# Optimization experiments

Measured on AMD Instinct MI355X. Metric: run time of the kernel, lower is better.

The kernel has to match this reference:

```python
import jax, jax.numpy as jnp
from jax import lax
import numpy as np

B, NUM_TPM, NUM_CNV, NODE_DIM, DRUG_FEAT = 32, 16000, 16000, 36, 75
N_DRUGS, N_ATOMS, N_PAIRS = 128, 64, 4096


def setup_inputs() -> dict:
    key = jax.random.key(0)
    ks = jax.random.split(key, 32)

    def w(k, shape):
        fan_in = shape[0] if len(shape) == 2 else int(np.prod(shape[1:]))
        return (jax.random.normal(k, shape, jnp.float32) / np.float32(np.sqrt(fan_in))).astype(jnp.float32)

    pic_dim = jax.random.normal(ks[0], (B, 3, 256, 256), jnp.float32)
    rna_seq = jax.random.normal(ks[1], (B, NUM_TPM), jnp.float32)
    gene_cnv = jax.random.normal(ks[2], (B, NUM_CNV), jnp.float32)
    drug_fea = jax.random.uniform(ks[3], (N_DRUGS, N_ATOMS, DRUG_FEAT), jnp.float32)
    a = (jax.random.uniform(ks[4], (N_DRUGS, N_ATOMS, N_ATOMS)) < 0.15).astype(jnp.float32)
    drug_adj = jnp.maximum(a, jnp.transpose(a, (0, 2, 1)))
    index_list = jnp.stack([
        jax.random.randint(ks[5], (N_PAIRS,), 0, B),
        jax.random.randint(ks[6], (N_PAIRS,), 0, N_DRUGS)], axis=1)
    target = jax.random.randint(ks[7], (N_PAIRS,), 0, 2)
    logit_scale = jnp.asarray(10.0, jnp.float32)
    return dict(
        pic_dim=pic_dim, rna_seq=rna_seq, gene_cnv=gene_cnv,
        drug_fea=drug_fea, drug_adj=drug_adj, index_list=index_list,
        target=target, logit_scale=logit_scale,
        conv_w=w(ks[8], (32, 3, 5, 5)), conv_b=jnp.zeros((32,), jnp.float32),
        fc1_w=w(ks[9], (32 * 128 * 128, 1024)), fc1_b=jnp.zeros((1024,), jnp.float32),
        fc2_w=w(ks[10], (1024, 36)), fc2_b=jnp.zeros((36,), jnp.float32),
        mlp1_w1=w(ks[11], (NUM_TPM, NUM_TPM // 4)), mlp1_b1=jnp.zeros((NUM_TPM // 4,), jnp.float32),
        mlp1_w2=w(ks[12], (NUM_TPM // 4, NODE_DIM)), mlp1_b2=jnp.zeros((NODE_DIM,), jnp.float32),
        mlp2_w1=w(ks[13], (NUM_CNV, NUM_CNV // 4)), mlp2_b1=jnp.zeros((NUM_CNV // 4,), jnp.float32),
        mlp2_w2=w(ks[14], (NUM_CNV // 4, NODE_DIM)), mlp2_b2=jnp.zeros((NODE_DIM,), jnp.float32),
        att_w1=w(ks[15], (36, 128)), att_b1=jnp.zeros((128,), jnp.float32),
        att_w2=w(ks[16], (128, 1)),
        end_w1=w(ks[17], (NODE_DIM * 4, NODE_DIM)), end_b1=jnp.zeros((NODE_DIM,), jnp.float32),
        end_w2=w(ks[18], (NODE_DIM, 2)), end_b2=jnp.zeros((2,), jnp.float32),
        gcn_w=w(ks[19], (DRUG_FEAT, NODE_DIM * 8)), gcn_w2=w(ks[20], (NODE_DIM * 8, NODE_DIM * 2)))


def _mlp(x, w1, b1, w2, b2):  # Linear-ReLU-(Dropout eval)-Linear-Softmax
    h = jax.nn.relu(x @ w1 + b1)
    return jax.nn.softmax(h @ w2 + b2, axis=-1)


def _ce(logits, labels):  # mean cross entropy, labels int [N]
    lp = jax.nn.log_softmax(logits, axis=-1)
    return -jnp.take_along_axis(lp, labels[:, None], axis=1).mean()


def reference(pic_dim, rna_seq, gene_cnv, drug_fea, drug_adj, index_list, target,
              logit_scale, conv_w, conv_b, fc1_w, fc1_b, fc2_w, fc2_b,
              mlp1_w1, mlp1_b1, mlp1_w2, mlp1_b2, mlp2_w1, mlp2_b1, mlp2_w2, mlp2_b2,
              att_w1, att_b1, att_w2, end_w1, end_b1, end_w2, end_b2, gcn_w, gcn_w2):
    # omics branches
    rna1 = _mlp(rna_seq, mlp1_w1, mlp1_b1, mlp1_w2, mlp1_b2)    # [B,36]
    cnv1 = _mlp(gene_cnv, mlp2_w1, mlp2_b1, mlp2_w2, mlp2_b2)   # [B,36]
    # image branch: conv(3->32,k5,p2) + relu + maxpool2 + fc
    x = lax.conv_general_dilated(pic_dim, conv_w, (1, 1), [(2, 2), (2, 2)])
    x = jax.nn.relu(x + conv_b[None, :, None, None])
    x = lax.reduce_window(x, -jnp.inf, lax.max, (1, 1, 2, 2), (1, 1, 2, 2), 'VALID')
    x = x.reshape(x.shape[0], -1)                               # [B, 32*128*128]
    x = jax.nn.relu(x @ fc1_w + fc1_b)
    pic1 = x @ fc2_w + fc2_b                                    # [B,36]
    # semantic attention over the two omics views
    z = jnp.stack([rna1, cnv1], axis=1)                         # [B,2,36]
    wv = (jnp.tanh(z @ att_w1 + att_b1) @ att_w2).mean(0)       # [2,1]
    beta = jax.nn.softmax(wv, axis=0)
    cell = (beta[None] * z).sum(1)                              # [B,36]
    # CLIP-style loss
    pic1 = pic1 / jnp.linalg.norm(pic1, axis=1, keepdims=True)
    cell = cell / jnp.linalg.norm(cell, axis=1, keepdims=True)
    image_fea = logit_scale * (pic1 @ cell.T)
    labels = jnp.arange(image_fea.shape[0])
    total_loss2 = (_ce(image_fea, labels) + _ce(image_fea.T, labels)) / 2
    cell_cat = jnp.concatenate([cell, pic1], axis=1)            # [B,72]
    # batched drug GCN (replaces per-drug python loop)
    eye = jnp.eye(N_ATOMS, dtype=jnp.float32)
    def gcn_one(X, A):
        Ht = A.T * (1.0 - eye) + eye        # set diagonal to 1 (add self loops)
        deg = Ht.sum(1)
        dinv = jnp.where(deg == 0, 0.0, 1.0 / deg)
        Hn = dinv[:, None] * Ht             # D^-1 A_hat  (== H.t() after norm)
        out = Hn @ ((Hn @ (X @ gcn_w)) @ gcn_w2)
        return jnp.max(jax.nn.relu(out), axis=0)  # max over atoms -> [72]
    drugfea = jax.vmap(gcn_one)(drug_fea, drug_adj)             # [n_drugs,72]
    # pair prediction head
    Bc = jnp.concatenate([cell_cat[index_list[:, 0]], drugfea[index_list[:, 1]]], axis=1)
    Bp = _mlp(Bc, end_w1, end_b1, end_w2, end_b2)               # [n_pairs,2]
    loss1 = _ce(Bp, target)
    return (loss1, total_loss2, Bp, target)
```

## Files before the change

### kernel.cpp

```cpp
#include <hip/hip_runtime.h>
#include <hip/hip_bf16.h>
#include <math.h>

typedef float evf4 __attribute__((ext_vector_type(4)));

__device__ __forceinline__ void fma4(float4& a, float s, const float4& v) {
  a.x += s * v.x; a.y += s * v.y; a.z += s * v.z; a.w += s * v.w;
}
__device__ __forceinline__ void fadd4(float4& a, const float4& v) {
  a.x += v.x; a.y += v.y; a.z += v.z; a.w += v.w;
}
__device__ __forceinline__ float4 ntload4(const float4* p) {
  evf4 v = __builtin_nontemporal_load((const evf4*)p);
  return make_float4(v.x, v.y, v.z, v.w);
}

__device__ __forceinline__ void conv_body(
    const float* __restrict__ pic, const float* __restrict__ cw,
    const float* __restrict__ cb, float* __restrict__ pooled,
    int bid, float tile[3][8][260]) {
  int php = bid & 63, ocg2 = (bid >> 6) & 1, b = bid >> 7;
  int tid = threadIdx.x;
  int pw = tid & 127, phl = tid >> 7;
  int ph = php * 2 + phl;
  int h_base = php * 4 - 2;
  for (int i = tid; i < 3 * 8 * 260; i += 256) {
    int c = i % 260; int rr = (i / 260) & 7; int ic = i / (260 * 8);
    int h = h_base + rr, w = c - 2;
    float v = 0.f;
    if (h >= 0 && h < 256 && w >= 0 && w < 256)
      v = pic[((size_t)b * 3 + ic) * 65536 + h * 256 + w];
    tile[ic][rr][c] = v;
  }
  __syncthreads();
  float acc[16][4];
#pragma unroll
  for (int o = 0; o < 16; ++o)
#pragma unroll
    for (int q = 0; q < 4; ++q) acc[o][q] = 0.f;
  int r0 = phl * 2;
  int c0 = pw * 2;
#pragma unroll
  for (int ic = 0; ic < 3; ++ic) {
    float win[6][6];
#pragma unroll
    for (int r = 0; r < 6; ++r)
#pragma unroll
      for (int cc = 0; cc < 6; ++cc) win[r][cc] = tile[ic][r0 + r][c0 + cc];
#pragma unroll
    for (int o = 0; o < 16; ++o) {
      const float* __restrict__ wk = cw + ((ocg2 * 16 + o) * 3 + ic) * 25;
#pragma unroll
      for (int kh = 0; kh < 5; ++kh)
#pragma unroll
        for (int kw = 0; kw < 5; ++kw) {
          float wv = wk[kh * 5 + kw];
          acc[o][0] += win[kh][kw] * wv;
          acc[o][1] += win[kh][kw + 1] * wv;
          acc[o][2] += win[kh + 1][kw] * wv;
          acc[o][3] += win[kh + 1][kw + 1] * wv;
        }
    }
  }
#pragma unroll
  for (int o = 0; o < 16; ++o) {
    float m = fmaxf(fmaxf(acc[o][0], acc[o][1]), fmaxf(acc[o][2], acc[o][3]));
    m = fmaxf(m + cb[ocg2 * 16 + o], 0.f);
    pooled[(((size_t)b * 32 + ocg2 * 16 + o) * 128 + ph) * 128 + pw] = m;
  }
}

__device__ __forceinline__ void wc_body(
    const float* __restrict__ w1, const float* __restrict__ w2,
    float* __restrict__ wc, int bx) {
  int i = bx * 256 + threadIdx.x;
  if (i >= 75 * 72) return;
  int r = i / 72, c = i - r * 72;
  float s = 0.f;
  for (int k = 0; k < 288; ++k) s += w1[r * 288 + k] * w2[k * 72 + c];
  wc[i] = s;
}

__global__ __launch_bounds__(256) void k1_conv_wc_kernel(
    const float* __restrict__ pic, const float* __restrict__ cw,
    const float* __restrict__ cb, float* __restrict__ pooled,
    const float* __restrict__ gw, const float* __restrict__ gw2,
    float* __restrict__ wcb) {
  __shared__ float tile[3][8][260];
  int bid = blockIdx.x;
  if (bid < 4096) conv_body(pic, cw, cb, pooled, bid, tile);
  else            wc_body(gw, gw2, wcb, bid - 4096);
}

__device__ __forceinline__ void gemm32p_body(
    const float* __restrict__ X, const float* __restrict__ W,
    float* __restrict__ partial, int K, int N, int chunk,
    int bx, int split, float xs[128][36]) {
  int tid = threadIdx.x;
  int colv = bx * 256 + tid;
  int col0 = colv * 4;
  bool active = col0 < N;
  int k0 = split * chunk, k1 = min(k0 + chunk, K);
  size_t Nv = (size_t)(N >> 2);
  const float4* Wv = (const float4*)W;
  float4 acc[32];
#pragma unroll
  for (int b = 0; b < 32; ++b) acc[b] = make_float4(0.f, 0.f, 0.f, 0.f);

  float4 xpre[4];
#pragma unroll
  for (int j = 0; j < 4; ++j) {
    int idx = tid + j * 256;
    int b = idx >> 5, kk = (idx & 31) * 4;
    xpre[j] = *(const float4*)&X[(size_t)b * K + k0 + kk];
  }

  auto fmablk = [&](int kk, const float4& w4) {
    const float4* xr = (const float4*)xs[kk];
#pragma unroll
    for (int b4 = 0; b4 < 8; ++b4) {
      float4 xv = xr[b4];
      fma4(acc[b4 * 4 + 0], xv.x, w4);
      fma4(acc[b4 * 4 + 1], xv.y, w4);
      fma4(acc[b4 * 4 + 2], xv.z, w4);
      fma4(acc[b4 * 4 + 3], xv.w, w4);
    }
  };

  for (int kt = k0; kt < k1; kt += 128) {
    __syncthreads();
#pragma unroll
    for (int j = 0; j < 4; ++j) {
      int idx = tid + j * 256;
      int b = idx >> 5, kk = (idx & 31) * 4;
      xs[kk + 0][b] = xpre[j].x;
      xs[kk + 1][b] = xpre[j].y;
      xs[kk + 2][b] = xpre[j].z;
      xs[kk + 3][b] = xpre[j].w;
    }
    __syncthreads();
    if (kt + 128 < k1) {
#pragma unroll
      for (int j = 0; j < 4; ++j) {
        int idx = tid + j * 256;
        int b = idx >> 5, kk = (idx & 31) * 4;
        xpre[j] = *(const float4*)&X[(size_t)b * K + kt + 128 + kk];
      }
    }
    if (active) {
      const float4* wp = Wv + (size_t)kt * Nv + colv;
      float4 cur[8], nxt[8];
#pragma unroll
      for (int j = 0; j < 8; ++j) cur[j] = ntload4(wp + (size_t)j * Nv);
#pragma unroll 1
      for (int g = 0; g < 15; ++g) {
        const float4* wn = wp + 8 * Nv;
#pragma unroll
        for (int j = 0; j < 8; ++j) nxt[j] = ntload4(wn + (size_t)j * Nv);
        int kb = g * 8;
#pragma unroll
        for (int j = 0; j < 8; ++j) fmablk(kb + j, cur[j]);
#pragma unroll
        for (int j = 0; j < 8; ++j) cur[j] = nxt[j];
        wp = wn;
      }
#pragma unroll
      for (int j = 0; j < 8; ++j) fmablk(120 + j, cur[j]);
    }
  }
  if (active) {
    float* p = partial + (size_t)split * 32 * N + col0;
#pragma unroll
    for (int b = 0; b < 32; ++b) *(float4*)(p + (size_t)b * N) = acc[b];
  }
}

__global__ __launch_bounds__(256) void gemm_all_kernel(
    const float* __restrict__ pooled, const float* __restrict__ fc1w,
    float* __restrict__ pfc1,
    const float* __restrict__ rna, const float* __restrict__ m1w1, float* __restrict__ pm1,
    const float* __restrict__ cnv, const float* __restrict__ m2w1, float* __restrict__ pm2) {
  __shared__ float xs[128][36];
  int b = blockIdx.x;
  if (b < 512) {
    gemm32p_body(pooled, fc1w, pfc1, 524288, 1024, 1024, 0, b, xs);
  } else {
    int j = b - 512;
    int z = j / 252;
    int r = j % 252;
    int bx = r & 3, split = r >> 2;
    if (z == 0) gemm32p_body(rna, m1w1, pm1, 16000, 4000, 256, bx, split, xs);
    else        gemm32p_body(cnv, m2w1, pm2, 16000, 4000, 256, bx, split, xs);
  }
}

__device__ __forceinline__ void reduce_s1_body(
    const float* __restrict__ partial, float* __restrict__ p2,
    int bx, int sy) {
  int i = bx * 256 + threadIdx.x;
  const float4* p = (const float4*)partial + (size_t)(sy * 128) * 8192 + i;
  const size_t st = 8192;
  float4 s0 = make_float4(0, 0, 0, 0), s1 = s0, s2 = s0, s3 = s0;
  for (int sp = 0; sp < 128; sp += 4) {
    fadd4(s0, ntload4(p + (sp + 0) * st));
    fadd4(s1, ntload4(p + (sp + 1) * st));
    fadd4(s2, ntload4(p + (sp + 2) * st));
    fadd4(s3, ntload4(p + (sp + 3) * st));
  }
  float4 r;
  r.x = (s0.x + s1.x) + (s2.x + s3.x);
  r.y = (s0.y + s1.y) + (s2.y + s3.y);
  r.z = (s0.z + s1.z) + (s2.z + s3.z);
  r.w = (s0.w + s1.w) + (s2.w + s3.w);
  ((float4*)p2)[(size_t)sy * 8192 + i] = r;
}

__device__ __forceinline__ void reduce_mlp_body(
    const float* __restrict__ partial, const float* __restrict__ bias,
    float* __restrict__ out, int bx) {
  int i = bx * 256 + threadIdx.x;
  if (i >= 32000) return;
  const float4* p = (const float4*)partial + i;
  const size_t st = 32000;
  float4 s0 = make_float4(0, 0, 0, 0), s1 = s0, s2 = s0, s3 = s0;
  int sp = 0;
  for (; sp + 4 <= 63; sp += 4) {
    fadd4(s0, ntload4(p + (sp + 0) * st));
    fadd4(s1, ntload4(p + (sp + 1) * st));
    fadd4(s2, ntload4(p + (sp + 2) * st));
    fadd4(s3, ntload4(p + (sp + 3) * st));
  }
  for (; sp < 63; ++sp) fadd4(s0, ntload4(p + (size_t)sp * st));
  float4 bi = ((const float4*)bias)[i % 1000];
  float4 r;
  r.x = fmaxf(bi.x + (s0.x + s1.x) + (s2.x + s3.x), 0.f);
  r.y = fmaxf(bi.y + (s0.y + s1.y) + (s2.y + s3.y), 0.f);
  r.z = fmaxf(bi.z + (s0.z + s1.z) + (s2.z + s3.z), 0.f);
  r.w = fmaxf(bi.w + (s0.w + s1.w) + (s2.w + s3.w), 0.f);
  ((float4*)out)[i] = r;
}

__global__ __launch_bounds__(256) void k3_reduce_kernel(
    const float* __restrict__ pfc1, float* __restrict__ p2fc1,
    const float* __restrict__ pm1, const float* __restrict__ m1b1, float* __restrict__ h1,
    const float* __restrict__ pm2, const float* __restrict__ m2b1, float* __restrict__ h2) {
  int b = blockIdx.x;
  if (b < 128) {
    reduce_s1_body(pfc1, p2fc1, b & 31, b >> 5);
  } else {
    int idx = b - 128;
    if (idx < 125) reduce_mlp_body(pm1, m1b1, h1, idx);
    else           reduce_mlp_body(pm2, m2b1, h2, idx - 125);
  }
}

__device__ __forceinline__ void reduce_s2_body(
    const float* __restrict__ p2, const float* __restrict__ bias,
    float* __restrict__ out, int bx) {
  int i = bx * 256 + threadIdx.x;
  float4 a = ((const float4*)p2)[i];
  float4 b = ((const float4*)p2)[8192 + i];
  float4 c = ((const float4*)p2)[16384 + i];
  float4 d = ((const float4*)p2)[24576 + i];
  float4 bi = ((const float4*)bias)[i & 255];
  float4 r;
  r.x = fmaxf(bi.x + (a.x + b.x) + (c.x + d.x), 0.f);
  r.y = fmaxf(bi.y + (a.y + b.y) + (c.y + d.y), 0.f);
  r.z = fmaxf(bi.z + (a.z + b.z) + (c.z + d.z), 0.f);
  r.w = fmaxf(bi.w + (a.w + b.w) + (c.w + d.w), 0.f);
  ((float4*)out)[i] = r;
}

__device__ __forceinline__ void gcn_body(
    const float* __restrict__ Xg, const float* __restrict__ Ag,
    const float* __restrict__ Wc, float* __restrict__ drugfea, int d,
    float Hn[64][65], float Xs[64][75], float Wcs[75][72],
    float Ys[64][72], float Ts[64][72]) {
  int tid = threadIdx.x;
  const float* Ad = Ag + (size_t)d * 4096;
  const float* Xd = Xg + (size_t)d * 4800;
  for (int i = tid; i < 4096; i += 256) {
    int r = i & 63, c = i >> 6;
    Hn[r][c] = (r == c) ? 1.f : Ad[c * 64 + r];
  }
  for (int i = tid; i < 4800; i += 256) Xs[i / 75][i % 75] = Xd[i];
  for (int i = tid; i < 5400; i += 256) Wcs[i / 72][i % 72] = Wc[i];
  __syncthreads();
  if (tid < 64) {
    float s = 0.f;
    for (int c = 0; c < 64; ++c) s += Hn[tid][c];
    float inv = (s == 0.f) ? 0.f : 1.f / s;
    for (int c = 0; c < 64; ++c) Hn[tid][c] *= inv;
  }
  __syncthreads();
  int rb = tid >> 3, cb = tid & 7;
  int r0 = rb * 2, c0 = cb * 9;
  {
    float o0[9], o1[9];
#pragma unroll
    for (int j = 0; j < 9; ++j) { o0[j] = 0.f; o1[j] = 0.f; }
    for (int k = 0; k < 75; ++k) {
      float x0 = Xs[r0][k], x1 = Xs[r0 + 1][k];
#pragma unroll
      for (int j = 0; j < 9; ++j) {
        float w = Wcs[k][c0 + j];
        o0[j] += x0 * w; o1[j] += x1 * w;
      }
    }
#pragma unroll
    for (int j = 0; j < 9; ++j) { Ys[r0][c0 + j] = o0[j]; Ys[r0 + 1][c0 + j] = o1[j]; }
  }
  __syncthreads();
  {
    float o0[9], o1[9];
#pragma unroll
    for (int j = 0; j < 9; ++j) { o0[j] = 0.f; o1[j] = 0.f; }
    for (int k = 0; k < 64; ++k) {
      float x0 = Hn[r0][k], x1 = Hn[r0 + 1][k];
#pragma unroll
      for (int j = 0; j < 9; ++j) {
        float w = Ys[k][c0 + j];
        o0[j] += x0 * w; o1[j] += x1 * w;
      }
    }
#pragma unroll
    for (int j = 0; j < 9; ++j) { Ts[r0][c0 + j] = o0[j]; Ts[r0 + 1][c0 + j] = o1[j]; }
  }
  __syncthreads();
  {
    float o0[9], o1[9];
#pragma unroll
    for (int j = 0; j < 9; ++j) { o0[j] = 0.f; o1[j] = 0.f; }
    for (int k = 0; k < 64; ++k) {
      float x0 = Hn[r0][k], x1 = Hn[r0 + 1][k];
#pragma unroll
      for (int j = 0; j < 9; ++j) {
        float w = Ts[k][c0 + j];
        o0[j] += x0 * w; o1[j] += x1 * w;
      }
    }
#pragma unroll
    for (int j = 0; j < 9; ++j) {
      Ys[r0][c0 + j] = fmaxf(o0[j], 0.f);
      Ys[r0 + 1][c0 + j] = fmaxf(o1[j], 0.f);
    }
  }
  __syncthreads();
  if (tid < 72) {
    float m = Ys[0][tid];
    for (int i = 1; i < 64; ++i) m = fmaxf(m, Ys[i][tid]);
    drugfea[d * 72 + tid] = m;
  }
}

__global__ __launch_bounds__(256) void k4_s2_gcn_kernel(
    const float* __restrict__ p2fc1, const float* __restrict__ fc1_b,
    float* __restrict__ fcact,
    const float* __restrict__ Xg, const float* __restrict__ Ag,
    const float* __restrict__ wcb, float* __restrict__ drugfea) {
  __shared__ float Hn[64][65];
  __shared__ float Xs[64][75];
  __shared__ float Wcs[75][72];
  __shared__ float Ys[64][72];
  __shared__ float Ts[64][72];
  int b = blockIdx.x;
  if (b < 32) reduce_s2_body(p2fc1, fc1_b, fcact, b);
  else        gcn_body(Xg, Ag, wcb, drugfea, b - 32, Hn, Xs, Wcs, Ys, Ts);
}

__global__ __launch_bounds__(256) void lin36_all_kernel(
    const float* __restrict__ X0, const float* __restrict__ W0,
    const float* __restrict__ bi0, float* __restrict__ out0,
    const float* __restrict__ X1, const float* __restrict__ W1,
    const float* __restrict__ bi1, float* __restrict__ out1,
    const float* __restrict__ X2, const float* __restrict__ W2,
    const float* __restrict__ bi2, float* __restrict__ out2) {
  const float* X; const float* W; const float* bias; float* out; int K; bool do_sm;
  if (blockIdx.y == 0)      { X = X0; W = W0; bias = bi0; out = out0; K = 4000; do_sm = true; }
  else if (blockIdx.y == 1) { X = X1; W = W1; bias = bi1; out = out1; K = 4000; do_sm = true; }
  else                      { X = X2; W = W2; bias = bi2; out = out2; K = 1024; do_sm = false; }
  __shared__ float xs[4000];
  __shared__ float red[28][36];
  __shared__ float vals[36];
  __shared__ float mxv, smv;
  int b = blockIdx.x, tid = threadIdx.x;
  for (int i = tid; i < K; i += 256) xs[i] = X[(size_t)b * K + i];
  __syncthreads();
  if (tid < 252) {
    int c4 = tid % 9, g = tid / 9;
    const float4* W4 = (const float4*)W;
    float4 s = make_float4(0.f, 0.f, 0.f, 0.f);
    for (int k = g; k < K; k += 28) fma4(s, xs[k], W4[k * 9 + c4]);
    red[g][c4 * 4 + 0] = s.x; red[g][c4 * 4 + 1] = s.y;
    red[g][c4 * 4 + 2] = s.z; red[g][c4 * 4 + 3] = s.w;
  }
  __syncthreads();
  if (tid < 36) {
    float s = bias[tid];
    for (int g = 0; g < 28; ++g) s += red[g][tid];
    vals[tid] = s;
  }
  __syncthreads();
  if (do_sm) {
    if (tid == 0) {
      float m = -1e30f;
      for (int j = 0; j < 36; ++j) m = fmaxf(m, vals[j]);
      float e = 0.f;
      for (int j = 0; j < 36; ++j) e += expf(vals[j] - m);
      mxv = m; smv = e;
    }
    __syncthreads();
    if (tid < 36) out[b * 36 + tid] = expf(vals[tid] - mxv) / smv;
  } else {
    if (tid < 36) out[b * 36 + tid] = vals[tid];
  }
}

__global__ __launch_bounds__(256) void head_kernel(
    const float* __restrict__ rna1, const float* __restrict__ cnv1,
    const float* __restrict__ pic1r, const float* __restrict__ aw1,
    const float* __restrict__ ab1, const float* __restrict__ aw2,
    const float* __restrict__ scale_p, float* __restrict__ cell_cat,
    float* __restrict__ dout) {
  __shared__ float z[2][32][36];
  __shared__ float pic1n[32][36];
  __shared__ float celln[32][36];
  __shared__ float fea[32][32];
  __shared__ float wvp[64];
  __shared__ float beta0, beta1;
  __shared__ float rowl[32], coll[32];
  int tid = threadIdx.x;
  for (int i = tid; i < 1152; i += 256) {
    int b = i / 36, k = i - (i / 36) * 36;
    z[0][b][k] = rna1[i];
    z[1][b][k] = cnv1[i];
    pic1n[b][k] = pic1r[i];
  }
  __syncthreads();
  {
    int p = tid >> 2, sub = tid & 3;
    int b = p >> 1, v = p & 1;
    float s = 0.f;
    for (int h = sub; h < 128; h += 4) {
      float a = ab1[h];
      for (int k = 0; k < 36; ++k) a += z[v][b][k] * aw1[k * 128 + h];
      s += tanhf(a) * aw2[h];
    }
    s += __shfl_down(s, 1, 64);
    s += __shfl_down(s, 2, 64);
    if (sub == 0) wvp[p] = s;
  }
  __syncthreads();
  if (tid == 0) {
    float w0 = 0.f, w1 = 0.f;
    for (int b = 0; b < 32; ++b) { w0 += wvp[b * 2]; w1 += wvp[b * 2 + 1]; }
    w0 /= 32.f; w1 /= 32.f;
    float m = fmaxf(w0, w1);
    float e0 = expf(w0 - m), e1 = expf(w1 - m);
    beta0 = e0 / (e0 + e1); beta1 = e1 / (e0 + e1);
  }
  __syncthreads();
  for (int i = tid; i < 1152; i += 256) {
    int b = i / 36, k = i - (i / 36) * 36;
    celln[b][k] = beta0 * z[0][b][k] + beta1 * z[1][b][k];
  }
  __syncthreads();
  if (tid < 32) {
    float s = 0.f;
    for (int k = 0; k < 36; ++k) { float x = pic1n[tid][k]; s += x * x; }
    float inv = 1.f / sqrtf(s);
    for (int k = 0; k < 36; ++k) pic1n[tid][k] *= inv;
  } else if (tid < 64) {
    int b = tid - 32;
    float s = 0.f;
    for (int k = 0; k < 36; ++k) { float x = celln[b][k]; s += x * x; }
    float inv = 1.f / sqrtf(s);
    for (int k = 0; k < 36; ++k) celln[b][k] *= inv;
  }
  __syncthreads();
  for (int i = tid; i < 1152; i += 256) {
    int b = i / 36, k = i - (i / 36) * 36;
    cell_cat[b * 72 + k] = celln[b][k];
    cell_cat[b * 72 + 36 + k] = pic1n[b][k];
  }
  float sc = *scale_p;
  for (int t = tid; t < 1024; t += 256) {
    int i = t >> 5, j = t & 31;
    float s = 0.f;
    for (int k = 0; k < 36; ++k) s += pic1n[i][k] * celln[j][k];
    fea[i][j] = sc * s;
  }
  __syncthreads();
  if (tid < 32) {
    float m = -1e30f;
    for (int j = 0; j < 32; ++j) m = fmaxf(m, fea[tid][j]);
    float e = 0.f;
    for (int j = 0; j < 32; ++j) e += expf(fea[tid][j] - m);
    rowl[tid] = (logf(e) + m) - fea[tid][tid];
  } else if (tid < 64) {
    int j = tid - 32;
    float m = -1e30f;
    for (int i = 0; i < 32; ++i) m = fmaxf(m, fea[i][j]);
    float e = 0.f;
    for (int i = 0; i < 32; ++i) e += expf(fea[i][j] - m);
    coll[j] = (logf(e) + m) - fea[j][j];
  }
  __syncthreads();
  if (tid == 0) {
    float s1 = 0.f, s2 = 0.f;
    for (int i = 0; i < 32; ++i) { s1 += rowl[i]; s2 += coll[i]; }
    dout[1] = 0.5f * (s1 / 32.f + s2 / 32.f);
  }
}

__global__ __launch_bounds__(256) void pair_kernel(
    const float* __restrict__ cell_cat, const float* __restrict__ drugfea,
    const int* __restrict__ idx, const int* __restrict__ target,
    const float* __restrict__ w1, const float* __restrict__ b1,
    const float* __restrict__ w2, const float* __restrict__ b2,
    float* __restrict__ bp_out, float* __restrict__ tgt_out,
    float* __restrict__ blocksums) {
  __shared__ float w1s[144][36];
  __shared__ float ccs[32][73];
  __shared__ float dfs[128][73];
  __shared__ float w2s[72], b2s[2];
  __shared__ float lsum[256];
  int tid = threadIdx.x;
  {
    float4* dst = (float4*)&w1s[0][0];
    const float4* src = (const float4*)w1;
    for (int i = tid; i < 1296; i += 256) dst[i] = src[i];
  }
  for (int i = tid; i < 2304; i += 256) ccs[i / 72][i % 72] = cell_cat[i];
  for (int i = tid; i < 9216; i += 256) dfs[i / 72][i % 72] = drugfea[i];
  if (tid < 72) w2s[tid] = w2[tid];
  if (tid < 2) b2s[tid] = b2[tid];
  __syncthreads();
  int p = blockIdx.x * 256 + tid;
  int ci = idx[p * 2], dj = idx[p * 2 + 1];
  float4 h4[9];
  {
    const float4* bb = (const float4*)b1;
#pragma unroll
    for (int q = 0; q < 9; ++q) h4[q] = bb[q];
  }
  for (int k = 0; k < 72; ++k) {
    float x = ccs[ci][k];
    const float4* wr = (const float4*)&w1s[k][0];
#pragma unroll
    for (int q = 0; q < 9; ++q) fma4(h4[q], x, wr[q]);
  }
  for (int k = 0; k < 72; ++k) {
    float x = dfs[dj][k];
    const float4* wr = (const float4*)&w1s[72 + k][0];
#pragma unroll
    for (int q = 0; q < 9; ++q) fma4(h4[q], x, wr[q]);
  }
  float l0 = b2s[0], l1 = b2s[1];
#pragma unroll
  for (int q = 0; q < 9; ++q) {
    float hv;
    hv = fmaxf(h4[q].x, 0.f); l0 += hv * w2s[(q * 4 + 0) * 2]; l1 += hv * w2s[(q * 4 + 0) * 2 + 1];
    hv = fmaxf(h4[q].y, 0.f); l0 += hv * w2s[(q * 4 + 1) * 2]; l1 += hv * w2s[(q * 4 + 1) * 2 + 1];
    hv = fmaxf(h4[q].z, 0.f); l0 += hv * w2s[(q * 4 + 2) * 2]; l1 += hv * w2s[(q * 4 + 2) * 2 + 1];
    hv = fmaxf(h4[q].w, 0.f); l0 += hv * w2s[(q * 4 + 3) * 2]; l1 += hv * w2s[(q * 4 + 3) * 2 + 1];
  }
  float m = fmaxf(l0, l1);
  float e0 = expf(l0 - m), e1 = expf(l1 - m);
  float inv = 1.f / (e0 + e1);
  float p0 = e0 * inv, p1 = e1 * inv;
  bp_out[p * 2] = p0;
  bp_out[p * 2 + 1] = p1;
  int t = target[p];
  float mm = fmaxf(p0, p1);
  float lse = logf(expf(p0 - mm) + expf(p1 - mm)) + mm;
  float chosen = t ? p1 : p0;
  lsum[tid] = lse - chosen;
  tgt_out[p] = (float)t;
  __syncthreads();
  for (int s = 128; s > 0; s >>= 1) {
    if (tid < s) lsum[tid] += lsum[tid + s];
    __syncthreads();
  }
  if (tid == 0) blocksums[blockIdx.x] = lsum[0];
}

__global__ void final_kernel(const float* __restrict__ blocksums, float* __restrict__ dout) {
  if (threadIdx.x == 0 && blockIdx.x == 0) {
    float s = 0.f;
    for (int i = 0; i < 16; ++i) s += blocksums[i];
    dout[0] = s / 4096.f;
  }
}

extern "C" void kernel_launch(void* const* d_in, const int* in_sizes, int n_in,
                              void* d_out, int out_size, void* d_ws, size_t ws_size,
                              hipStream_t stream) {
  (void)in_sizes; (void)n_in; (void)out_size; (void)ws_size;
  const float* pic        = (const float*)d_in[0];
  const float* rna        = (const float*)d_in[1];
  const float* cnv        = (const float*)d_in[2];
  const float* drug_fea   = (const float*)d_in[3];
  const float* drug_adj   = (const float*)d_in[4];
  const int*   index_list = (const int*)d_in[5];
  const int*   target     = (const int*)d_in[6];
  const float* logit_scale= (const float*)d_in[7];
  const float* conv_w     = (const float*)d_in[8];
  const float* conv_b     = (const float*)d_in[9];
  const float* fc1_w      = (const float*)d_in[10];
  const float* fc1_b      = (const float*)d_in[11];
  const float* fc2_w      = (const float*)d_in[12];
  const float* fc2_b      = (const float*)d_in[13];
  const float* m1w1       = (const float*)d_in[14];
  const float* m1b1       = (const float*)d_in[15];
  const float* m1w2       = (const float*)d_in[16];
  const float* m1b2       = (const float*)d_in[17];
  const float* m2w1       = (const float*)d_in[18];
  const float* m2b1       = (const float*)d_in[19];
  const float* m2w2       = (const float*)d_in[20];
  const float* m2b2       = (const float*)d_in[21];
  const float* aw1        = (const float*)d_in[22];
  const float* ab1        = (const float*)d_in[23];
  const float* aw2        = (const float*)d_in[24];
  const float* ew1        = (const float*)d_in[25];
  const float* eb1        = (const float*)d_in[26];
  const float* ew2        = (const float*)d_in[27];
  const float* eb2        = (const float*)d_in[28];
  const float* gw         = (const float*)d_in[29];
  const float* gw2        = (const float*)d_in[30];

  float* ws = (float*)d_ws;
  float* pooled  = ws;
  float* pfc1    = ws + 16777216;
  float* p2fc1   = ws + 33554432;
  float* pm1     = ws + 33685504;
  float* pm2     = ws + 41749504;
  float* fcact   = ws + 49813504;
  float* h1      = ws + 49846272;
  float* h2      = ws + 49974272;
  float* rna1    = ws + 50102272;
  float* cnv1    = ws + 50103424;
  float* pic1r   = ws + 50104576;
  float* wcb     = ws + 50105728;
  float* drugf   = ws + 50111128;
  float* cellcat = ws + 50120344;
  float* bsums   = ws + 50122648;

  float* out = (float*)d_out;

  k1_conv_wc_kernel<<<4118, 256, 0, stream>>>(pic, conv_w, conv_b, pooled,
                                              gw, gw2, wcb);
  gemm_all_kernel<<<1016, 256, 0, stream>>>(pooled, fc1_w, pfc1,
                                            rna, m1w1, pm1, cnv, m2w1, pm2);
  k3_reduce_kernel<<<378, 256, 0, stream>>>(pfc1, p2fc1,
                                            pm1, m1b1, h1, pm2, m2b1, h2);
  k4_s2_gcn_kernel<<<160, 256, 0, stream>>>(p2fc1, fc1_b, fcact,
                                            drug_fea, drug_adj, wcb, drugf);
  {
    dim3 g(32, 3);
    lin36_all_kernel<<<g, 256, 0, stream>>>(h1, m1w2, m1b2, rna1,
                                            h2, m2w2, m2b2, cnv1,
                                            fcact, fc2_w, fc2_b, pic1r);
  }
  head_kernel<<<1, 256, 0, stream>>>(rna1, cnv1, pic1r, aw1, ab1, aw2,
                                     logit_scale, cellcat, out);
  pair_kernel<<<16, 256, 0, stream>>>(cellcat, drugf, index_list, target,
                                      ew1, eb1, ew2, eb2,
                                      out + 2, out + 2 + 8192, bsums);
  final_kernel<<<1, 64, 0, stream>>>(bsums, out);
}
```

Before: 1.007 ms.

## Co-schedule MLP GEMMs with conv in one launch, split fc1 GEMM out

Moves the two large 16000x4000 MLP first-layer GEMMs, which do not depend on the conv output, into the conv+wc kernel so they run alongside the convolution. The fc1 GEMM, which needs the pooled conv output, becomes its own launch. The aim is to overlap the bandwidth-heavy MLP weight streaming with the compute-heavy conv and so shorten the critical path. The fused kernel shares one shared-memory buffer sized for the conv tile, and block ordering places the GEMM blocks first so they start early.

```diff
diff --git a/kernel.cpp b/kernel.cpp
--- a/kernel.cpp
+++ b/kernel.cpp
@@ -81,17 +81,6 @@
   wc[i] = s;
 }
 
-__global__ __launch_bounds__(256) void k1_conv_wc_kernel(
-    const float* __restrict__ pic, const float* __restrict__ cw,
-    const float* __restrict__ cb, float* __restrict__ pooled,
-    const float* __restrict__ gw, const float* __restrict__ gw2,
-    float* __restrict__ wcb) {
-  __shared__ float tile[3][8][260];
-  int bid = blockIdx.x;
-  if (bid < 4096) conv_body(pic, cw, cb, pooled, bid, tile);
-  else            wc_body(gw, gw2, wcb, bid - 4096);
-}
-
 __device__ __forceinline__ void gemm32p_body(
     const float* __restrict__ X, const float* __restrict__ W,
     float* __restrict__ partial, int K, int N, int chunk,
@@ -175,23 +164,34 @@
   }
 }
 
-__global__ __launch_bounds__(256) void gemm_all_kernel(
-    const float* __restrict__ pooled, const float* __restrict__ fc1w,
-    float* __restrict__ pfc1,
+__global__ __launch_bounds__(256) void k1_fused_kernel(
+    const float* __restrict__ pic, const float* __restrict__ cw,
+    const float* __restrict__ cb, float* __restrict__ pooled,
+    const float* __restrict__ gw, const float* __restrict__ gw2,
+    float* __restrict__ wcb,
     const float* __restrict__ rna, const float* __restrict__ m1w1, float* __restrict__ pm1,
     const float* __restrict__ cnv, const float* __restrict__ m2w1, float* __restrict__ pm2) {
-  __shared__ float xs[128][36];
+  __shared__ __align__(16) float smem[3 * 8 * 260];
   int b = blockIdx.x;
-  if (b < 512) {
-    gemm32p_body(pooled, fc1w, pfc1, 524288, 1024, 1024, 0, b, xs);
-  } else {
-    int j = b - 512;
-    int z = j / 252;
-    int r = j % 252;
+  if (b < 504) {
+    float (*xs)[36] = (float(*)[36])smem;
+    int z = b / 252;
+    int r = b % 252;
     int bx = r & 3, split = r >> 2;
     if (z == 0) gemm32p_body(rna, m1w1, pm1, 16000, 4000, 256, bx, split, xs);
     else        gemm32p_body(cnv, m2w1, pm2, 16000, 4000, 256, bx, split, xs);
-  }
+  } else if (b < 526) {
+    wc_body(gw, gw2, wcb, b - 504);
+  } else {
+    conv_body(pic, cw, cb, pooled, b - 526, (float(*)[8][260])smem);
+  }
+}
+
+__global__ __launch_bounds__(256) void gemm_fc1_kernel(
+    const float* __restrict__ pooled, const float* __restrict__ fc1w,
+    float* __restrict__ pfc1) {
+  __shared__ float xs[128][36];
+  gemm32p_body(pooled, fc1w, pfc1, 524288, 1024, 1024, 0, blockIdx.x, xs);
 }
 
 __device__ __forceinline__ void reduce_s1_body(
@@ -648,10 +648,10 @@
 
   float* out = (float*)d_out;
 
-  k1_conv_wc_kernel<<<4118, 256, 0, stream>>>(pic, conv_w, conv_b, pooled,
-                                              gw, gw2, wcb);
-  gemm_all_kernel<<<1016, 256, 0, stream>>>(pooled, fc1_w, pfc1,
+  k1_fused_kernel<<<4622, 256, 0, stream>>>(pic, conv_w, conv_b, pooled,
+                                            gw, gw2, wcb,
                                             rna, m1w1, pm1, cnv, m2w1, pm2);
+  gemm_fc1_kernel<<<512, 256, 0, stream>>>(pooled, fc1_w, pfc1);
   k3_reduce_kernel<<<378, 256, 0, stream>>>(pfc1, p2fc1,
                                             pm1, m1b1, h1, pm2, m2b1, h2);
   k4_s2_gcn_kernel<<<160, 256, 0, stream>>>(p2fc1, fc1_b, fcact,
```

Result: slower. 1.130 ms (+12.3%).
